# Kernel tuning notes

Hardware: AMD Instinct MI355X
Metric: run time of the kernel (lower is better)

The kernel has to match this reference:

```python
import jax, jax.numpy as jnp
import numpy as np

N_NODES = 50000
N_EDGES = 800000
HID = 64
OUT = 64
REL = 5


def setup_inputs() -> dict:
    key = jax.random.key(0)
    ks = jax.random.split(key, 9)
    s_in = 1.0 / np.sqrt(HID)
    return {
        "contagion_risk": jax.random.normal(ks[0], (N_NODES, HID), jnp.float32),
        "edge_weight": jax.random.uniform(ks[1], (N_EDGES,), jnp.float32),
        # torch Linear weights stored transposed as [in, out] so y = x @ W + b
        "W_in_w": jax.random.uniform(ks[2], (HID, HID), jnp.float32, -s_in, s_in),
        "W_in_b": jax.random.uniform(ks[3], (HID,), jnp.float32, -s_in, s_in),
        "W_rel": jax.random.uniform(ks[4], (REL, HID, HID), jnp.float32, -s_in, s_in),
        "W_out_w": jax.random.uniform(ks[5], (HID, OUT), jnp.float32, -s_in, s_in),
        "W_out_b": jax.random.uniform(ks[6], (OUT,), jnp.float32, -s_in, s_in),
        "edge_index": jax.random.randint(ks[7], (2, N_EDGES), 0, N_NODES, jnp.int64 if jax.config.jax_enable_x64 else jnp.int32),
        "edge_type": jax.random.randint(ks[8], (N_EDGES,), 0, REL, jnp.int32),
        "num_nodes": N_NODES,
    }


def _dan_forward(contagion_risk, W_in_w, W_in_b, W_rel, W_out_w, W_out_b,
                 edge_index, edge_type, num_nodes):
    row, col = edge_index[0], edge_index[1]  # dst, src
    x = contagion_risk @ W_in_w + W_in_b                       # [N, H]
    x_j = x[col]                                               # [E, H] gather

    # gcn_norm (no self loops, unit edge weights): deg over col
    ones = jnp.ones(col.shape[0], x.dtype)
    deg = jax.ops.segment_sum(ones, col, num_segments=num_nodes)
    dis = jnp.where(deg > 0, jax.lax.rsqrt(jnp.maximum(deg, 1.0)), 0.0)
    norm_w = (dis[row] * dis[col])[:, None]                    # [E, 1]
    msg_gcn = jax.ops.segment_sum(x_j * norm_w, row, num_segments=num_nodes)

    # per-relation masked GEMM (grouped GEMM over REL relation types)
    res = jnp.zeros_like(x_j)
    for i in range(W_rel.shape[0]):
        mask = (edge_type == i)[:, None]
        res = res + jnp.where(mask, x_j @ W_rel[i], 0.0)

    # segment softmax over destination-node groups (per feature channel)
    seg_max = jax.ops.segment_max(res, row, num_segments=num_nodes)
    e = jnp.exp(res - seg_max[row])
    seg_sum = jax.ops.segment_sum(e, row, num_segments=num_nodes)
    weig = e / (seg_sum[row] + 1e-16)

    msg = jax.ops.segment_sum(res * weig, row, num_segments=num_nodes)
    out = (msg_gcn + 0.5 * jax.nn.relu(msg)) @ W_out_w + W_out_b
    return out


def reference(contagion_risk, edge_weight, W_in_w, W_in_b, W_rel, W_out_w, W_out_b,
              edge_index, edge_type, num_nodes):
    # edge_weight is accepted by the original forward but never used
    return _dan_forward(contagion_risk, W_in_w, W_in_b, W_rel, W_out_w, W_out_b,
                        edge_index, edge_type, num_nodes)
```

## Files before the change

### kernel.cpp

```cpp
#include <hip/hip_runtime.h>
#include <hip/hip_bf16.h>

#define HID 64
#define REL 5
#define EPB 4096
#define BKT 256

typedef short bf16x8 __attribute__((ext_vector_type(8)));
typedef float f32x4 __attribute__((ext_vector_type(4)));

__device__ __forceinline__ float bf2f(unsigned short u) {
    return __uint_as_float(((unsigned)u) << 16);
}
__device__ __forceinline__ unsigned short f2bf(float f) {
    __hip_bfloat16 h = (__hip_bfloat16)f;
    return *(unsigned short*)&h;
}
__device__ __forceinline__ int det_f32(const unsigned short* __restrict__ wb) {
    int lane = threadIdx.x & 63;
    bool big = (lane < 32) ? (fabsf(bf2f(wb[2 * lane])) > 0.26f) : false;
    return (__ballot(big) != 0ull) ? 1 : 0;
}
__device__ __forceinline__ int det_i64(const int* __restrict__ ei) {
    int lane = threadIdx.x & 63;
    bool odd_nz = (ei[2 * lane + 1] != 0);
    return (__ballot(odd_nz) == 0ull) ? 1 : 0;
}
__device__ __forceinline__ void dec_edge(const int* __restrict__ ei, int i64,
                                         int E, int e, int& r, int& c) {
    if (i64) { r = ei[2 * e]; c = ei[2 * (E + e)]; }
    else     { r = ei[e];     c = ei[E + e]; }
}

__global__ void k_pack(const void* Win, const void* bin, const void* Wr,
                       const void* Wout, const void* bout,
                       unsigned short* __restrict__ Bpk,
                       float* __restrict__ binf, float* __restrict__ boutf) {
    int f = det_f32((const unsigned short*)bin);
    int gid = blockIdx.x * 256 + threadIdx.x;
    if (gid < 7 * 2 * 4 * 64) {
        int lane = gid & 63;
        int nt = (gid >> 6) & 3;
        int ks = (gid >> 8) & 1;
        int mat = gid >> 9;
        int q = lane >> 4, n = nt * 16 + (lane & 15);
#pragma unroll
        for (int j = 0; j < 8; j++) {
            int k = ks * 32 + q * 8 + j;
            int idx = k * 64 + n;
            float val;
            if (mat == 0)
                val = f ? ((const float*)Win)[idx] : bf2f(((const unsigned short*)Win)[idx]);
            else if (mat <= 5) {
                int ii = (mat - 1) * 4096 + idx;
                val = f ? ((const float*)Wr)[ii] : bf2f(((const unsigned short*)Wr)[ii]);
            } else
                val = f ? ((const float*)Wout)[idx] : bf2f(((const unsigned short*)Wout)[idx]);
            Bpk[(size_t)gid * 8 + j] = f2bf(val);
        }
    }
    if (gid < 64)
        binf[gid] = f ? ((const float*)bin)[gid] : bf2f(((const unsigned short*)bin)[gid]);
    else if (gid >= 64 && gid < 128) {
        int i = gid - 64;
        boutf[i] = f ? ((const float*)bout)[i] : bf2f(((const unsigned short*)bout)[i]);
    }
}

__global__ void k_p1a(const int* __restrict__ ei,
                      int* __restrict__ hist, int E, int NB, int nblk) {
    extern __shared__ int lh[];
    int i64 = det_i64(ei);
    int tid = threadIdx.x, blk = blockIdx.x;
    for (int i = tid; i < 2 * NB; i += 256) lh[i] = 0;
    __syncthreads();
#pragma unroll
    for (int k = 0; k < EPB / 256; k++) {
        int e = blk * EPB + k * 256 + tid;
        if (e < E) {
            int r, c;
            dec_edge(ei, i64, E, e, r, c);
            atomicAdd(&lh[r >> 8], 1);
            atomicAdd(&lh[NB + (c >> 8)], 1);
        }
    }
    __syncthreads();
    int NBn = NB * nblk;
    for (int i = tid; i < NB; i += 256) {
        hist[i * nblk + blk] = lh[i];
        hist[NBn + i * nblk + blk] = lh[NB + i];
    }
}

__global__ void s_blk(const int* __restrict__ v, int* __restrict__ bsum, int M) {
    __shared__ int red[256];
    int t = threadIdx.x;
    int i0 = blockIdx.x * 1024 + t * 4;
    int s = 0;
#pragma unroll
    for (int j = 0; j < 4; j++) { int i = i0 + j; if (i < M) s += v[i]; }
    red[t] = s;
    __syncthreads();
    for (int d = 128; d > 0; d >>= 1) {
        if (t < d) red[t] += red[t + d];
        __syncthreads();
    }
    if (t == 0) bsum[blockIdx.x] = red[0];
}

__global__ void s_apply(int* __restrict__ v, const int* __restrict__ bsum,
                        int M, int nsb) {
    __shared__ int red[256];
    int t = threadIdx.x, bk = blockIdx.x;
    int acc = 0;
    for (int i = t; i < nsb; i += 256)
        if (i < bk) acc += bsum[i];
    red[t] = acc;
    __syncthreads();
    for (int d = 128; d > 0; d >>= 1) {
        if (t < d) red[t] += red[t + d];
        __syncthreads();
    }
    int base = red[0];
    __syncthreads();
    int i0 = bk * 1024 + t * 4;
    int x[4];
    int s = 0;
#pragma unroll
    for (int j = 0; j < 4; j++) {
        int i = i0 + j;
        x[j] = (i < M) ? v[i] : 0;
        s += x[j];
    }
    red[t] = s;
    __syncthreads();
    for (int d = 1; d < 256; d <<= 1) {
        int add = (t >= d) ? red[t - d] : 0;
        __syncthreads();
        red[t] += add;
        __syncthreads();
    }
    int run = base + red[t] - s;
#pragma unroll
    for (int j = 0; j < 4; j++) {
        int i = i0 + j;
        if (i < M) { int tmp = x[j]; v[i] = run; run += tmp; }
    }
}

__global__ void k_p1c(const int* __restrict__ ei, const int* __restrict__ et,
                      const int* __restrict__ hist,
                      unsigned* __restrict__ rbuf, unsigned char* __restrict__ cb8,
                      int E, int NB, int nblk) {
    extern __shared__ int lh[];
    int i64 = det_i64(ei);
    int tid = threadIdx.x, blk = blockIdx.x;
    for (int i = tid; i < 2 * NB; i += 256) lh[i] = 0;
    __syncthreads();
    int NBn = NB * nblk;
#pragma unroll
    for (int k = 0; k < EPB / 256; k++) {
        int e = blk * EPB + k * 256 + tid;
        if (e < E) {
            int r, c;
            dec_edge(ei, i64, E, e, r, c);
            int t = et[e];
            int binR = r >> 8;
            int posR = hist[binR * nblk + blk] + atomicAdd(&lh[binR], 1);
            rbuf[posR] = ((unsigned)(r & 255) << 20) | ((unsigned)t << 17) | (unsigned)c;
            int binC = c >> 8;
            int posC = hist[NBn + binC * nblk + blk] - E + atomicAdd(&lh[NB + binC], 1);
            cb8[posC] = (unsigned char)(c & 255);
        }
    }
}

__global__ void k_p2(const unsigned* __restrict__ rbuf, const unsigned char* __restrict__ cb8,
                     const int* __restrict__ hist,
                     int* __restrict__ off, unsigned* __restrict__ edata4,
                     float* __restrict__ dis, int E, int N, int NB, int nblk) {
    __shared__ int lcnt[BKT], excl[BKT], lcnt2[BKT];
    int tid = threadIdx.x;
    int bk = blockIdx.x;
    if (bk < NB) {
        int bstart = hist[bk * nblk];
        int bend = (bk + 1 < NB) ? hist[(bk + 1) * nblk] : E;
        lcnt[tid] = 0; lcnt2[tid] = 0;
        __syncthreads();
        for (int e = bstart + tid; e < bend; e += 256)
            atomicAdd(&lcnt[(rbuf[e] >> 20) & 255], 1);
        __syncthreads();
        int s = lcnt[tid];
        excl[tid] = s;
        __syncthreads();
        for (int d = 1; d < 256; d <<= 1) {
            int add = (tid >= d) ? excl[tid - d] : 0;
            __syncthreads();
            excl[tid] += add;
            __syncthreads();
        }
        int base = excl[tid] - s;
        excl[tid] = base;
        __syncthreads();
        int node = bk * BKT + tid;
        if (node < N) off[node] = bstart + base;
        if (bk == 0 && tid == 0) off[N] = E;
        for (int e = bstart + tid; e < bend; e += 256) {
            unsigned rec = rbuf[e];
            int rl = (rec >> 20) & 255;
            int t = (rec >> 17) & 7;
            int c = rec & 0x1FFFF;
            int pos = bstart + excl[rl] + atomicAdd(&lcnt2[rl], 1);
            edata4[pos] = (unsigned)c | ((unsigned)t << 20);
        }
    } else {
        int bk2 = bk - NB;
        int NBn = NB * nblk;
        int cstart = hist[NBn + bk2 * nblk] - E;
        int cend = (bk2 + 1 < NB) ? hist[NBn + (bk2 + 1) * nblk] - E : E;
        lcnt[tid] = 0;
        __syncthreads();
        for (int e = cstart + tid; e < cend; e += 256)
            atomicAdd(&lcnt[cb8[e]], 1);
        __syncthreads();
        int node = bk2 * BKT + tid;
        int d = lcnt[tid];
        dis[node] = (d > 0) ? rsqrtf((float)d) : 0.f;
    }
}

__device__ __forceinline__ bf16x8 load_a8(const void* A, int f, size_t base) {
    if (f) {
        const float* Af = (const float*)A + base;
        bf16x8 r;
#pragma unroll
        for (int j = 0; j < 8; j++) r[j] = (short)f2bf(Af[j]);
        return r;
    }
    return *(const bf16x8*)((const unsigned short*)A + base);
}

__global__ void __launch_bounds__(256)
k_xy(const void* __restrict__ A, const void* __restrict__ binp,
     const unsigned short* __restrict__ Bpk,
     const float* __restrict__ binf, const float* __restrict__ dis,
     unsigned short* __restrict__ Yi, int N, int Np) {
    __shared__ unsigned short Bs[6 * 2 * 4 * 64 * 8];
    __shared__ unsigned short Xs[64 * 64];
    __shared__ unsigned short Xss[64 * 64];
    __shared__ unsigned short Ys[64 * 64];
    __shared__ float bs[64];
    int f = det_f32((const unsigned short*)binp);
    int tid = threadIdx.x;
    for (int i = tid; i < 6 * 2 * 4 * 64; i += 256)
        ((uint4*)Bs)[i] = ((const uint4*)Bpk)[i];
    if (tid < 64) bs[tid] = binf[tid];
    __syncthreads();

    int w = tid >> 6, lane = tid & 63;
    int q = lane >> 4, n16 = lane & 15;
    int mrow = w * 16 + n16;
    int arow = min(blockIdx.x * 64 + mrow, N - 1);
    bf16x8 a0 = load_a8(A, f, (size_t)arow * 64 + 8 * q);
    bf16x8 a1 = load_a8(A, f, (size_t)arow * 64 + 8 * q + 32);

    float disv[4];
#pragma unroll
    for (int r = 0; r < 4; r++) {
        int node = blockIdx.x * 64 + w * 16 + 4 * q + r;
        disv[r] = dis[node];
    }

    size_t snode = (size_t)(blockIdx.x * 64 + mrow);

#pragma unroll
    for (int nt = 0; nt < 4; nt++) {
        f32x4 d = {0.f, 0.f, 0.f, 0.f};
        bf16x8 b0 = *(const bf16x8*)(Bs + (size_t)(((0 * 2 + 0) * 4 + nt) * 64 + lane) * 8);
        bf16x8 b1 = *(const bf16x8*)(Bs + (size_t)(((0 * 2 + 1) * 4 + nt) * 64 + lane) * 8);
        d = __builtin_amdgcn_mfma_f32_16x16x32_bf16(a0, b0, d, 0, 0, 0);
        d = __builtin_amdgcn_mfma_f32_16x16x32_bf16(a1, b1, d, 0, 0, 0);
        int col = nt * 16 + n16;
#pragma unroll
        for (int r = 0; r < 4; r++) {
            int rowl = w * 16 + 4 * q + r;
            float xval = d[r] + bs[col];
            Xs[rowl * 64 + col] = f2bf(xval);
            Xss[rowl * 64 + col] = f2bf(xval * disv[r]);
        }
    }
    bf16x8 a20 = *(const bf16x8*)(Xs + mrow * 64 + 8 * q);
    bf16x8 a21 = *(const bf16x8*)(Xs + mrow * 64 + 8 * q + 32);

    for (int rel = 0; rel < REL; rel++) {
        int mat = 1 + rel;
#pragma unroll
        for (int nt = 0; nt < 4; nt++) {
            f32x4 d = {0.f, 0.f, 0.f, 0.f};
            bf16x8 b0 = *(const bf16x8*)(Bs + (size_t)(((mat * 2 + 0) * 4 + nt) * 64 + lane) * 8);
            bf16x8 b1 = *(const bf16x8*)(Bs + (size_t)(((mat * 2 + 1) * 4 + nt) * 64 + lane) * 8);
            d = __builtin_amdgcn_mfma_f32_16x16x32_bf16(a20, b0, d, 0, 0, 0);
            d = __builtin_amdgcn_mfma_f32_16x16x32_bf16(a21, b1, d, 0, 0, 0);
            int col = nt * 16 + n16;
#pragma unroll
            for (int r = 0; r < 4; r++)
                Ys[(w * 16 + 4 * q + r) * 64 + col] = f2bf(d[r]);
        }
        unsigned short* dst = Yi + ((size_t)rel * Np + snode) * 128;
#pragma unroll
        for (int ch = 0; ch < 2; ch++) {
            int c0 = 8 * q + 32 * ch;
            bf16x8 y8 = *(const bf16x8*)(Ys + mrow * 64 + c0);
            bf16x8 x8 = *(const bf16x8*)(Xss + mrow * 64 + c0);
            bf16x8 lo, hi;
#pragma unroll
            for (int j = 0; j < 4; j++) {
                lo[2 * j] = y8[j];     lo[2 * j + 1] = x8[j];
                hi[2 * j] = y8[4 + j]; hi[2 * j + 1] = x8[4 + j];
            }
            *(bf16x8*)(dst + 2 * c0)     = lo;
            *(bf16x8*)(dst + 2 * c0 + 8) = hi;
        }
    }
}

__global__ void __launch_bounds__(256)
k_main(const unsigned short* __restrict__ Yi, const int* __restrict__ off,
       const unsigned* __restrict__ edata4, const float* __restrict__ dis,
       unsigned short* __restrict__ v, int N, int Np) {
    int tid = threadIdx.x;
    int wv = tid >> 6, lane = tid & 63;
    int n = blockIdx.x * 4 + wv;
    if (n >= N) return;
    int half = lane >> 5;
    int co = (lane & 31) * 4;
    int e0 = off[n], e1 = off[n + 1];
    float s0 = 0.f, s1 = 0.f, u0 = 0.f, u1 = 0.f, g0 = 0.f, g1 = 0.f;
    float s0b = 0.f, s1b = 0.f, u0b = 0.f, u1b = 0.f, g0b = 0.f, g1b = 0.f;

    int e = e0 + half;
    for (; e + 6 < e1; e += 8) {
        unsigned md[4];
#pragma unroll
        for (int j = 0; j < 4; j++) md[j] = edata4[e + 2 * j];
        uint2 y[4];
#pragma unroll
        for (int j = 0; j < 4; j++) {
            int c = md[j] & 0xFFFFF, t = md[j] >> 20;
            y[j] = *(const uint2*)(Yi + ((size_t)t * Np + c) * 128 + co);
        }
#pragma unroll
        for (int j = 0; j < 4; j++) {
            float r0 = __uint_as_float(y[j].x << 16);
            float r1 = __uint_as_float(y[j].y << 16);
            float p0 = __expf(fminf(r0, 60.f));
            float p1 = __expf(fminf(r1, 60.f));
            if (j & 1) {
                g0b += __uint_as_float(y[j].x & 0xFFFF0000u);
                g1b += __uint_as_float(y[j].y & 0xFFFF0000u);
                s0b += p0; s1b += p1;
                u0b += r0 * p0; u1b += r1 * p1;
            } else {
                g0 += __uint_as_float(y[j].x & 0xFFFF0000u);
                g1 += __uint_as_float(y[j].y & 0xFFFF0000u);
                s0 += p0; s1 += p1;
                u0 += r0 * p0; u1 += r1 * p1;
            }
        }
    }
    for (; e < e1; e += 2) {
        unsigned md = edata4[e];
        int c = md & 0xFFFFF, t = md >> 20;
        uint2 ya = *(const uint2*)(Yi + ((size_t)t * Np + c) * 128 + co);
        float r0 = __uint_as_float(ya.x << 16);
        float r1 = __uint_as_float(ya.y << 16);
        g0 += __uint_as_float(ya.x & 0xFFFF0000u);
        g1 += __uint_as_float(ya.y & 0xFFFF0000u);
        float p0 = __expf(fminf(r0, 60.f));
        float p1 = __expf(fminf(r1, 60.f));
        s0 += p0; s1 += p1;
        u0 += r0 * p0; u1 += r1 * p1;
    }
    s0 += s0b; s1 += s1b; u0 += u0b; u1 += u1b; g0 += g0b; g1 += g1b;

    s0 += __shfl_xor(s0, 32); s1 += __shfl_xor(s1, 32);
    u0 += __shfl_xor(u0, 32); u1 += __shfl_xor(u1, 32);
    g0 += __shfl_xor(g0, 32); g1 += __shfl_xor(g1, 32);
    if (half == 0) {
        float dn = dis[n];
        float m0 = u0 / (s0 + 1e-16f), m1 = u1 / (s1 + 1e-16f);
        float v0 = g0 * dn + 0.5f * fmaxf(m0, 0.f);
        float v1 = g1 * dn + 0.5f * fmaxf(m1, 0.f);
        unsigned pack = (unsigned)f2bf(v0) | ((unsigned)f2bf(v1) << 16);
        *(unsigned*)(v + (size_t)n * 64 + (lane & 31) * 2) = pack;
    }
}

__global__ void __launch_bounds__(256)
k_out(const unsigned short* __restrict__ v, const void* __restrict__ binp,
      const unsigned short* __restrict__ Bpk,
      const float* __restrict__ boutf, void* __restrict__ outv, int N, int Np) {
    __shared__ unsigned short Bs[2 * 4 * 64 * 8];
    __shared__ float Os[64 * 64];
    __shared__ float bs[64];
    int f = det_f32((const unsigned short*)binp);
    int tid = threadIdx.x;
    const unsigned short* src = Bpk + (size_t)6 * 2 * 4 * 64 * 8;
    for (int i = tid; i < 2 * 4 * 64; i += 256)
        ((uint4*)Bs)[i] = ((const uint4*)src)[i];
    if (tid < 64) bs[tid] = boutf[tid];
    __syncthreads();

    int w = tid >> 6, lane = tid & 63;
    int q = lane >> 4, n16 = lane & 15;
    int mrow = w * 16 + n16;
    int arow = min(blockIdx.x * 64 + mrow, N - 1);
    bf16x8 a0 = *(const bf16x8*)(v + (size_t)arow * 64 + 8 * q);
    bf16x8 a1 = *(const bf16x8*)(v + (size_t)arow * 64 + 8 * q + 32);
#pragma unroll
    for (int nt = 0; nt < 4; nt++) {
        f32x4 d = {0.f, 0.f, 0.f, 0.f};
        bf16x8 b0 = *(const bf16x8*)(Bs + (size_t)((0 * 4 + nt) * 64 + lane) * 8);
        bf16x8 b1 = *(const bf16x8*)(Bs + (size_t)((1 * 4 + nt) * 64 + lane) * 8);
        d = __builtin_amdgcn_mfma_f32_16x16x32_bf16(a0, b0, d, 0, 0, 0);
        d = __builtin_amdgcn_mfma_f32_16x16x32_bf16(a1, b1, d, 0, 0, 0);
        int col = nt * 16 + n16;
#pragma unroll
        for (int r = 0; r < 4; r++)
            Os[(w * 16 + 4 * q + r) * 64 + col] = d[r] + bs[col];
    }
    int node = blockIdx.x * 64 + mrow;
    if (node < N) {
        if (f) {
            float* dst = (float*)outv + (size_t)node * 64;
#pragma unroll
            for (int cchunk = 0; cchunk < 2; cchunk++) {
                int c0 = 8 * q + 32 * cchunk;
                *(f32x4*)(dst + c0)     = *(const f32x4*)(Os + mrow * 64 + c0);
                *(f32x4*)(dst + c0 + 4) = *(const f32x4*)(Os + mrow * 64 + c0 + 4);
            }
        } else {
            unsigned short* dst = (unsigned short*)outv + (size_t)node * 64;
#pragma unroll
            for (int cchunk = 0; cchunk < 2; cchunk++) {
                int c0 = 8 * q + 32 * cchunk;
                bf16x8 pk;
#pragma unroll
                for (int j = 0; j < 8; j++)
                    pk[j] = (short)f2bf(Os[mrow * 64 + c0 + j]);
                *(bf16x8*)(dst + c0) = pk;
            }
        }
    }
}

extern "C" void kernel_launch(void* const* d_in, const int* in_sizes, int n_in,
                              void* d_out, int out_size, void* d_ws, size_t ws_size,
                              hipStream_t stream) {
    const void* A    = d_in[0];
    const void* Win  = d_in[2];
    const void* bin  = d_in[3];
    const void* Wrel = d_in[4];
    const void* Wout = d_in[5];
    const void* bout = d_in[6];
    const int* ei = (const int*)d_in[7];
    const int* et = (const int*)d_in[8];
    int N = in_sizes[0] / HID;
    int E = in_sizes[8];
    int Np = ((N + BKT - 1) / BKT) * BKT;
    int NB = Np / BKT;
    int nblk = (E + EPB - 1) / EPB;
    int M = 2 * NB * nblk;
    int nsb = (M + 1023) / 1024;

    char* p = (char*)d_ws;
    auto carve = [&](size_t bytes) {
        char* q = p;
        p += (bytes + 15) & ~(size_t)15;
        return q;
    };
    unsigned short* Yi   = (unsigned short*)carve((size_t)REL * Np * 128 * 2);
    unsigned short* vv   = (unsigned short*)carve((size_t)Np * 64 * 2);
    unsigned*       rbuf = (unsigned*)carve((size_t)E * 4);
    unsigned char*  cb8  = (unsigned char*)carve((size_t)E);
    unsigned*       edata4 = (unsigned*)carve((size_t)E * 4);
    int*            hist = (int*)carve((size_t)M * 4);
    unsigned short* Bpk  = (unsigned short*)carve((size_t)7 * 4096 * 2);
    float* binf  = (float*)carve(64 * 4);
    float* boutf = (float*)carve(64 * 4);
    int* off     = (int*)carve((size_t)(N + 1) * 4);
    float* dis   = (float*)carve((size_t)Np * 4);
    int* bsum    = (int*)carve((size_t)nsb * 4);

    size_t lds_part = (size_t)2 * NB * 4;

    k_pack<<<14, 256, 0, stream>>>(Win, bin, Wrel, Wout, bout, Bpk, binf, boutf);
    k_p1a<<<nblk, 256, lds_part, stream>>>(ei, hist, E, NB, nblk);
    s_blk<<<nsb, 256, 0, stream>>>(hist, bsum, M);
    s_apply<<<nsb, 256, 0, stream>>>(hist, bsum, M, nsb);
    k_p1c<<<nblk, 256, lds_part, stream>>>(ei, et, hist, rbuf, cb8, E, NB, nblk);
    k_p2<<<2 * NB, 256, 0, stream>>>(rbuf, cb8, hist, off, edata4, dis, E, N, NB, nblk);
    k_xy<<<Np / 64, 256, 0, stream>>>(A, bin, Bpk, binf, dis, Yi, N, Np);
    k_main<<<(N + 3) / 4, 256, 0, stream>>>(Yi, off, edata4, dis, vv, N, Np);
    k_out<<<Np / 64, 256, 0, stream>>>(vv, bin, Bpk, boutf, d_out, N, Np);
}
```

Baseline: 194.9 us.

## Fuse output projection GEMM into edge aggregation kernel via LDS staging

Merges k_main and k_out so each block aggregates 64 nodes (16 per wave, processed sequentially) into an LDS tile, then applies the W_out MFMA and bias directly before writing the output. This removes one kernel launch and the round trip of the intermediate v buffer through global memory. In exchange the grid shrinks from about 12500 blocks to about 780, and each wave walks 16 nodes serially. That may reduce memory-level parallelism and occupancy for the latency-bound gather, and LDS use per block grows.

```diff
diff --git a/kernel.cpp b/kernel.cpp
--- a/kernel.cpp
+++ b/kernel.cpp
@@ -327,96 +327,93 @@
 __global__ void __launch_bounds__(256)
 k_main(const unsigned short* __restrict__ Yi, const int* __restrict__ off,
        const unsigned* __restrict__ edata4, const float* __restrict__ dis,
-       unsigned short* __restrict__ v, int N, int Np) {
+       const void* __restrict__ binp, const unsigned short* __restrict__ Bpk,
+       const float* __restrict__ boutf, void* __restrict__ outv, int N, int Np) {
+    __shared__ unsigned short Bs[2 * 4 * 64 * 8];
+    __shared__ unsigned short Vs[64 * 72];
+    __shared__ float Os[64 * 68];
+    __shared__ float bs[64];
+    int f = det_f32((const unsigned short*)binp);
     int tid = threadIdx.x;
-    int wv = tid >> 6, lane = tid & 63;
-    int n = blockIdx.x * 4 + wv;
-    if (n >= N) return;
+    const unsigned short* wsrc = Bpk + (size_t)6 * 2 * 4 * 64 * 8;
+    for (int i = tid; i < 2 * 4 * 64; i += 256)
+        ((uint4*)Bs)[i] = ((const uint4*)wsrc)[i];
+    if (tid < 64) bs[tid] = boutf[tid];
+    __syncthreads();
+
+    int w = tid >> 6, lane = tid & 63;
     int half = lane >> 5;
     int co = (lane & 31) * 4;
-    int e0 = off[n], e1 = off[n + 1];
-    float s0 = 0.f, s1 = 0.f, u0 = 0.f, u1 = 0.f, g0 = 0.f, g1 = 0.f;
-    float s0b = 0.f, s1b = 0.f, u0b = 0.f, u1b = 0.f, g0b = 0.f, g1b = 0.f;
-
-    int e = e0 + half;
-    for (; e + 6 < e1; e += 8) {
-        unsigned md[4];
-#pragma unroll
-        for (int j = 0; j < 4; j++) md[j] = edata4[e + 2 * j];
-        uint2 y[4];
-#pragma unroll
-        for (int j = 0; j < 4; j++) {
-            int c = md[j] & 0xFFFFF, t = md[j] >> 20;
-            y[j] = *(const uint2*)(Yi + ((size_t)t * Np + c) * 128 + co);
-        }
-#pragma unroll
-        for (int j = 0; j < 4; j++) {
-            float r0 = __uint_as_float(y[j].x << 16);
-            float r1 = __uint_as_float(y[j].y << 16);
-            float p0 = __expf(fminf(r0, 60.f));
-            float p1 = __expf(fminf(r1, 60.f));
-            if (j & 1) {
-                g0b += __uint_as_float(y[j].x & 0xFFFF0000u);
-                g1b += __uint_as_float(y[j].y & 0xFFFF0000u);
-                s0b += p0; s1b += p1;
-                u0b += r0 * p0; u1b += r1 * p1;
-            } else {
-                g0 += __uint_as_float(y[j].x & 0xFFFF0000u);
-                g1 += __uint_as_float(y[j].y & 0xFFFF0000u);
+    int n0 = blockIdx.x * 64 + w * 16;
+
+    for (int ln = 0; ln < 16; ln++) {
+        int n = n0 + ln;
+        float s0 = 0.f, s1 = 0.f, u0 = 0.f, u1 = 0.f, g0 = 0.f, g1 = 0.f;
+        float s0b = 0.f, s1b = 0.f, u0b = 0.f, u1b = 0.f, g0b = 0.f, g1b = 0.f;
+        if (n < N) {
+            int e0 = off[n], e1 = off[n + 1];
+            int e = e0 + half;
+            for (; e + 6 < e1; e += 8) {
+                unsigned md[4];
+#pragma unroll
+                for (int j = 0; j < 4; j++) md[j] = edata4[e + 2 * j];
+                uint2 y[4];
+#pragma unroll
+                for (int j = 0; j < 4; j++) {
+                    int c = md[j] & 0xFFFFF, t = md[j] >> 20;
+                    y[j] = *(const uint2*)(Yi + ((size_t)t * Np + c) * 128 + co);
+                }
+#pragma unroll
+                for (int j = 0; j < 4; j++) {
+                    float r0 = __uint_as_float(y[j].x << 16);
+                    float r1 = __uint_as_float(y[j].y << 16);
+                    float p0 = __expf(fminf(r0, 60.f));
+                    float p1 = __expf(fminf(r1, 60.f));
+                    if (j & 1) {
+                        g0b += __uint_as_float(y[j].x & 0xFFFF0000u);
+                        g1b += __uint_as_float(y[j].y & 0xFFFF0000u);
+                        s0b += p0; s1b += p1;
+                        u0b += r0 * p0; u1b += r1 * p1;
+                    } else {
+                        g0 += __uint_as_float(y[j].x & 0xFFFF0000u);
+                        g1 += __uint_as_float(y[j].y & 0xFFFF0000u);
+                        s0 += p0; s1 += p1;
+                        u0 += r0 * p0; u1 += r1 * p1;
+                    }
+                }
+            }
+            for (; e < e1; e += 2) {
+                unsigned md = edata4[e];
+                int c = md & 0xFFFFF, t = md >> 20;
+                uint2 ya = *(const uint2*)(Yi + ((size_t)t * Np + c) * 128 + co);
+                float r0 = __uint_as_float(ya.x << 16);
+                float r1 = __uint_as_float(ya.y << 16);
+                g0 += __uint_as_float(ya.x & 0xFFFF0000u);
+                g1 += __uint_as_float(ya.y & 0xFFFF0000u);
+                float p0 = __expf(fminf(r0, 60.f));
+                float p1 = __expf(fminf(r1, 60.f));
                 s0 += p0; s1 += p1;
                 u0 += r0 * p0; u1 += r1 * p1;
             }
         }
-    }
-    for (; e < e1; e += 2) {
-        unsigned md = edata4[e];
-        int c = md & 0xFFFFF, t = md >> 20;
-        uint2 ya = *(const uint2*)(Yi + ((size_t)t * Np + c) * 128 + co);
-        float r0 = __uint_as_float(ya.x << 16);
-        float r1 = __uint_as_float(ya.y << 16);
-        g0 += __uint_as_float(ya.x & 0xFFFF0000u);
-        g1 += __uint_as_float(ya.y & 0xFFFF0000u);
-        float p0 = __expf(fminf(r0, 60.f));
-        float p1 = __expf(fminf(r1, 60.f));
-        s0 += p0; s1 += p1;
-        u0 += r0 * p0; u1 += r1 * p1;
-    }
-    s0 += s0b; s1 += s1b; u0 += u0b; u1 += u1b; g0 += g0b; g1 += g1b;
-
-    s0 += __shfl_xor(s0, 32); s1 += __shfl_xor(s1, 32);
-    u0 += __shfl_xor(u0, 32); u1 += __shfl_xor(u1, 32);
-    g0 += __shfl_xor(g0, 32); g1 += __shfl_xor(g1, 32);
-    if (half == 0) {
-        float dn = dis[n];
-        float m0 = u0 / (s0 + 1e-16f), m1 = u1 / (s1 + 1e-16f);
-        float v0 = g0 * dn + 0.5f * fmaxf(m0, 0.f);
-        float v1 = g1 * dn + 0.5f * fmaxf(m1, 0.f);
-        unsigned pack = (unsigned)f2bf(v0) | ((unsigned)f2bf(v1) << 16);
-        *(unsigned*)(v + (size_t)n * 64 + (lane & 31) * 2) = pack;
-    }
-}
-
-__global__ void __launch_bounds__(256)
-k_out(const unsigned short* __restrict__ v, const void* __restrict__ binp,
-      const unsigned short* __restrict__ Bpk,
-      const float* __restrict__ boutf, void* __restrict__ outv, int N, int Np) {
-    __shared__ unsigned short Bs[2 * 4 * 64 * 8];
-    __shared__ float Os[64 * 64];
-    __shared__ float bs[64];
-    int f = det_f32((const unsigned short*)binp);
-    int tid = threadIdx.x;
-    const unsigned short* src = Bpk + (size_t)6 * 2 * 4 * 64 * 8;
-    for (int i = tid; i < 2 * 4 * 64; i += 256)
-        ((uint4*)Bs)[i] = ((const uint4*)src)[i];
-    if (tid < 64) bs[tid] = boutf[tid];
-    __syncthreads();
-
-    int w = tid >> 6, lane = tid & 63;
+        s0 += s0b; s1 += s1b; u0 += u0b; u1 += u1b; g0 += g0b; g1 += g1b;
+        s0 += __shfl_xor(s0, 32); s1 += __shfl_xor(s1, 32);
+        u0 += __shfl_xor(u0, 32); u1 += __shfl_xor(u1, 32);
+        g0 += __shfl_xor(g0, 32); g1 += __shfl_xor(g1, 32);
+        if (half == 0) {
+            float dn = (n < N) ? dis[n] : 0.f;
+            float m0 = u0 / (s0 + 1e-16f), m1 = u1 / (s1 + 1e-16f);
+            float v0 = g0 * dn + 0.5f * fmaxf(m0, 0.f);
+            float v1 = g1 * dn + 0.5f * fmaxf(m1, 0.f);
+            unsigned pack = (unsigned)f2bf(v0) | ((unsigned)f2bf(v1) << 16);
+            *(unsigned*)(Vs + (w * 16 + ln) * 72 + (lane & 31) * 2) = pack;
+        }
+    }
+
     int q = lane >> 4, n16 = lane & 15;
     int mrow = w * 16 + n16;
-    int arow = min(blockIdx.x * 64 + mrow, N - 1);
-    bf16x8 a0 = *(const bf16x8*)(v + (size_t)arow * 64 + 8 * q);
-    bf16x8 a1 = *(const bf16x8*)(v + (size_t)arow * 64 + 8 * q + 32);
+    bf16x8 a0 = *(const bf16x8*)(Vs + mrow * 72 + 8 * q);
+    bf16x8 a1 = *(const bf16x8*)(Vs + mrow * 72 + 8 * q + 32);
 #pragma unroll
     for (int nt = 0; nt < 4; nt++) {
         f32x4 d = {0.f, 0.f, 0.f, 0.f};
@@ -427,7 +424,7 @@
         int col = nt * 16 + n16;
 #pragma unroll
         for (int r = 0; r < 4; r++)
-            Os[(w * 16 + 4 * q + r) * 64 + col] = d[r] + bs[col];
+            Os[(w * 16 + 4 * q + r) * 68 + col] = d[r] + bs[col];
     }
     int node = blockIdx.x * 64 + mrow;
     if (node < N) {
@@ -436,8 +433,8 @@
 #pragma unroll
             for (int cchunk = 0; cchunk < 2; cchunk++) {
                 int c0 = 8 * q + 32 * cchunk;
-                *(f32x4*)(dst + c0)     = *(const f32x4*)(Os + mrow * 64 + c0);
-                *(f32x4*)(dst + c0 + 4) = *(const f32x4*)(Os + mrow * 64 + c0 + 4);
+                *(f32x4*)(dst + c0)     = *(const f32x4*)(Os + mrow * 68 + c0);
+                *(f32x4*)(dst + c0 + 4) = *(const f32x4*)(Os + mrow * 68 + c0 + 4);
             }
         } else {
             unsigned short* dst = (unsigned short*)outv + (size_t)node * 64;
@@ -447,7 +444,7 @@
                 bf16x8 pk;
 #pragma unroll
                 for (int j = 0; j < 8; j++)
-                    pk[j] = (short)f2bf(Os[mrow * 64 + c0 + j]);
+                    pk[j] = (short)f2bf(Os[mrow * 68 + c0 + j]);
                 *(bf16x8*)(dst + c0) = pk;
             }
         }
@@ -480,7 +477,6 @@
         return q;
     };
     unsigned short* Yi   = (unsigned short*)carve((size_t)REL * Np * 128 * 2);
-    unsigned short* vv   = (unsigned short*)carve((size_t)Np * 64 * 2);
     unsigned*       rbuf = (unsigned*)carve((size_t)E * 4);
     unsigned char*  cb8  = (unsigned char*)carve((size_t)E);
     unsigned*       edata4 = (unsigned*)carve((size_t)E * 4);
@@ -501,6 +497,6 @@
     k_p1c<<<nblk, 256, lds_part, stream>>>(ei, et, hist, rbuf, cb8, E, NB, nblk);
     k_p2<<<2 * NB, 256, 0, stream>>>(rbuf, cb8, hist, off, edata4, dis, E, N, NB, nblk);
     k_xy<<<Np / 64, 256, 0, stream>>>(A, bin, Bpk, binf, dis, Yi, N, Np);
-    k_main<<<(N + 3) / 4, 256, 0, stream>>>(Yi, off, edata4, dis, vv, N, Np);
-    k_out<<<Np / 64, 256, 0, stream>>>(vv, bin, Bpk, boutf, d_out, N, Np);
-}
+    k_main<<<Np / 64, 256, 0, stream>>>(Yi, off, edata4, dis, bin, Bpk, boutf,
+                                        d_out, N, Np);
+}
```

After: 218.5 us. 1.12x slower.
